# Performance work log

Hardware: AMD Instinct MI355X
Metric: run time of the kernel (lower is better)

## Reference

```python
import jax, jax.numpy as jnp
import numpy as np


def smooth_l1(x, y):
    d = jnp.abs(x - y)
    return jnp.where(d < 1.0, 0.5 * d * d, d - 0.5)


def setup_inputs() -> dict:
    key = jax.random.key(0)
    k1, k2, k3 = jax.random.split(key, 3)
    B, T, N, D = 4, 28, 1024, 3
    X_v = jax.random.normal(k1, (B, T, N, D), dtype=jnp.float32)
    target_X_v = jax.random.normal(k2, (B, T, N, D), dtype=jnp.float32)
    weights = jax.random.uniform(k3, (B, T), dtype=jnp.float32)
    return {"X_v": X_v, "target_X_v": target_X_v, "weights": weights}


def reference(X_v, target_X_v, weights):
    B = X_v.shape[0]
    # Pairwise squared distances [B,T,N,N] via ||p||^2 + ||t||^2 - 2 p.t
    pn = jnp.sum(X_v * X_v, axis=-1)                 # [B,T,N]
    tn = jnp.sum(target_X_v * target_X_v, axis=-1)   # [B,T,N]
    dist = (pn[..., :, None] + tn[..., None, :]
            - 2.0 * jnp.einsum('btnd,btmd->btnm', X_v, target_X_v))
    minv = jnp.argmin(dist, axis=-1)                 # [B,T,N] int
    # gather nearest target point for each pred point
    tagp = jnp.take_along_axis(target_X_v, minv[..., None], axis=2)  # [B,T,N,3]
    # per-(b,t) mean smooth-L1 over N points x 3 coords
    loss_bt = jnp.mean(smooth_l1(X_v, tagp), axis=(-2, -1))          # [B,T]
    loss = jnp.sum(loss_bt * weights) / B

    prec = jnp.mean(X_v, axis=2)        # [B,T,3]
    tarc = jnp.mean(target_X_v, axis=2) # [B,T,3]
    lossc = jnp.sum(smooth_l1(prec, tarc)) / (B * 3)
    return (loss, lossc)
```

## Files before the change

### kernel.cpp

```cpp
#include <hip/hip_runtime.h>

constexpr int Bc = 4;
constexpr int Tc = 28;
constexpr int Nc = 1024;
constexpr int Dc = 3;
constexpr int BT = Bc * Tc;
constexpr int QT = 256;

constexpr size_t WS_BESTV   = 0;
constexpr size_t WS_BESTI   = (size_t)BT * Nc * 4;
constexpr size_t WS_PARTIAL = WS_BESTI + (size_t)BT * Nc * 4;
constexpr size_t WS_PSUM    = WS_PARTIAL + 224;
constexpr size_t WS_TSUM    = WS_PSUM + BT * 2 * 3;

__device__ __forceinline__ float sl1(float d) {
    d = fabsf(d);
    return d < 1.0f ? 0.5f * d * d : d - 0.5f;
}

__global__ __launch_bounds__(256) void chamfer_quarter_kernel(
    const float* __restrict__ X, const float* __restrict__ Tg,
    float* __restrict__ bestv, int* __restrict__ besti,
    float* __restrict__ psum, float* __restrict__ tsum)
{
    __shared__ float4 sT4[QT];
    __shared__ float sred[4][3];

    const int bt  = blockIdx.x >> 3;
    const int ph  = (blockIdx.x >> 2) & 1;
    const int th  = blockIdx.x & 3;
    const int tid = threadIdx.x;

    const float* xb = X + (size_t)bt * (Nc * Dc);
    const int n0 = ph * 512 + tid;
    const int n1 = n0 + 256;
    const float pAx = xb[n0 * 3 + 0], pAy = xb[n0 * 3 + 1], pAz = xb[n0 * 3 + 2];
    const float pBx = xb[n1 * 3 + 0], pBy = xb[n1 * 3 + 1], pBz = xb[n1 * 3 + 2];

    if (tid < 64) {
        const float4* tg4 = (const float4*)(Tg + (size_t)bt * (Nc * Dc) + th * (QT * 3));
        const float4 r0 = tg4[3 * tid + 0];
        const float4 r1 = tg4[3 * tid + 1];
        const float4 r2 = tg4[3 * tid + 2];
        sT4[4 * tid + 0] = make_float4(r0.x, r0.y, r0.z, fmaf(r0.x, r0.x, fmaf(r0.y, r0.y, r0.z * r0.z)));
        sT4[4 * tid + 1] = make_float4(r0.w, r1.x, r1.y, fmaf(r0.w, r0.w, fmaf(r1.x, r1.x, r1.y * r1.y)));
        sT4[4 * tid + 2] = make_float4(r1.z, r1.w, r2.x, fmaf(r1.z, r1.z, fmaf(r1.w, r1.w, r2.x * r2.x)));
        sT4[4 * tid + 3] = make_float4(r2.y, r2.z, r2.w, fmaf(r2.y, r2.y, fmaf(r2.z, r2.z, r2.w * r2.w)));
        if (ph == 0) {
            float tx = r0.x + r0.w + r1.z + r2.y;
            float ty = r0.y + r1.x + r1.w + r2.z;
            float tz = r0.z + r1.y + r2.x + r2.w;
            #pragma unroll
            for (int off = 32; off; off >>= 1) {
                tx += __shfl_down(tx, off, 64);
                ty += __shfl_down(ty, off, 64);
                tz += __shfl_down(tz, off, 64);
            }
            if (tid == 0) {
                tsum[(bt * 4 + th) * 3 + 0] = tx;
                tsum[(bt * 4 + th) * 3 + 1] = ty;
                tsum[(bt * 4 + th) * 3 + 2] = tz;
            }
        }
    }
    __syncthreads();

    const float cA0 = -2.0f * pAx, cA1 = -2.0f * pAy, cA2 = -2.0f * pAz;
    const float cB0 = -2.0f * pBx, cB1 = -2.0f * pBy, cB2 = -2.0f * pBz;

    float bestA = 3.4e38f, bestB = 3.4e38f;
    int iA = 0, iB = 0;

    constexpr int PF = 8;
    float4 bufA[PF], bufB[PF];
    #pragma unroll
    for (int j = 0; j < PF; ++j) bufA[j] = sT4[j];

    for (int m0 = 0; m0 < QT; m0 += 2 * PF) {
        #pragma unroll
        for (int j = 0; j < PF; ++j) bufB[j] = sT4[m0 + PF + j];
        #pragma unroll
        for (int j = 0; j < PF; ++j) {
            const float4 t = bufA[j];
            const int m = m0 + j;
            float vA = fmaf(cA0, t.x, fmaf(cA1, t.y, fmaf(cA2, t.z, t.w)));
            float vB = fmaf(cB0, t.x, fmaf(cB1, t.y, fmaf(cB2, t.z, t.w)));
            bool ca = vA < bestA; bestA = ca ? vA : bestA; iA = ca ? m : iA;
            bool cb = vB < bestB; bestB = cb ? vB : bestB; iB = cb ? m : iB;
        }
        #pragma unroll
        for (int j = 0; j < PF; ++j) bufA[j] = sT4[(m0 + 2 * PF + j) & (QT - 1)];
        #pragma unroll
        for (int j = 0; j < PF; ++j) {
            const float4 t = bufB[j];
            const int m = m0 + PF + j;
            float vA = fmaf(cA0, t.x, fmaf(cA1, t.y, fmaf(cA2, t.z, t.w)));
            float vB = fmaf(cB0, t.x, fmaf(cB1, t.y, fmaf(cB2, t.z, t.w)));
            bool ca = vA < bestA; bestA = ca ? vA : bestA; iA = ca ? m : iA;
            bool cb = vB < bestB; bestB = cb ? vB : bestB; iB = cb ? m : iB;
        }
    }

    const size_t base = (size_t)bt * Nc;
    bestv[(base + n0) * 4 + th] = bestA;
    bestv[(base + n1) * 4 + th] = bestB;
    besti[(base + n0) * 4 + th] = th * QT + iA;
    besti[(base + n1) * 4 + th] = th * QT + iB;

    if (th == 0) {
        float sx = pAx + pBx, sy = pAy + pBy, sz = pAz + pBz;
        const int lane = tid & 63, wid = tid >> 6;
        #pragma unroll
        for (int off = 32; off; off >>= 1) {
            sx += __shfl_down(sx, off, 64);
            sy += __shfl_down(sy, off, 64);
            sz += __shfl_down(sz, off, 64);
        }
        if (lane == 0) { sred[wid][0] = sx; sred[wid][1] = sy; sred[wid][2] = sz; }
        __syncthreads();
        if (tid == 0) {
            #pragma unroll
            for (int k = 0; k < 3; ++k)
                psum[(bt * 2 + ph) * 3 + k] = sred[0][k] + sred[1][k] + sred[2][k] + sred[3][k];
        }
    }
}

__global__ __launch_bounds__(256) void gather_kernel(
    const float* __restrict__ X, const float* __restrict__ Tg,
    const float* __restrict__ W,
    const float4* __restrict__ bestv4, const int4* __restrict__ besti4,
    float* __restrict__ partial)
{
    __shared__ float sred[4];
    const int bt  = blockIdx.x >> 1;
    const int ph  = blockIdx.x & 1;
    const int tid = threadIdx.x;

    const float* xb = X  + (size_t)bt * (Nc * Dc);
    const float* tb = Tg + (size_t)bt * (Nc * Dc);
    const size_t base = (size_t)bt * Nc;

    float s = 0.0f;
    #pragma unroll
    for (int p = 0; p < 2; ++p) {
        const int n = ph * 512 + p * 256 + tid;
        const float4 bv = bestv4[base + n];
        const int4   bi = besti4[base + n];
        float best = bv.x; int idx = bi.x;
        if (bv.y < best) { best = bv.y; idx = bi.y; }
        if (bv.z < best) { best = bv.z; idx = bi.z; }
        if (bv.w < best) { best = bv.w; idx = bi.w; }
        const float px = xb[n * 3 + 0], py = xb[n * 3 + 1], pz = xb[n * 3 + 2];
        const float tx = tb[idx * 3 + 0], ty = tb[idx * 3 + 1], tz = tb[idx * 3 + 2];
        s += sl1(px - tx) + sl1(py - ty) + sl1(pz - tz);
    }

    const int lane = tid & 63, wid = tid >> 6;
    #pragma unroll
    for (int off = 32; off; off >>= 1) s += __shfl_down(s, off, 64);
    if (lane == 0) sred[wid] = s;
    __syncthreads();
    if (tid == 0)
        partial[blockIdx.x] = (sred[0] + sred[1] + sred[2] + sred[3]) * W[bt];
}

__global__ __launch_bounds__(256) void finalize_kernel(
    const float* __restrict__ ws, float* __restrict__ out)
{
    __shared__ float sred[4][2];
    const int tid = threadIdx.x;

    float lp = (tid < 224) ? ws[WS_PARTIAL + tid] : 0.0f;

    float lc = 0.0f;
    if (tid < BT) {
        const float inv = 1.0f / Nc;
        #pragma unroll
        for (int c = 0; c < 3; ++c) {
            float pm = (ws[WS_PSUM + (2 * tid) * 3 + c] + ws[WS_PSUM + (2 * tid + 1) * 3 + c]) * inv;
            float tm = (ws[WS_TSUM + (4 * tid) * 3 + c] + ws[WS_TSUM + (4 * tid + 1) * 3 + c]
                      + ws[WS_TSUM + (4 * tid + 2) * 3 + c] + ws[WS_TSUM + (4 * tid + 3) * 3 + c]) * inv;
            lc += sl1(pm - tm);
        }
    }

    const int lane = tid & 63, wid = tid >> 6;
    #pragma unroll
    for (int off = 32; off; off >>= 1) {
        lp += __shfl_down(lp, off, 64);
        lc += __shfl_down(lc, off, 64);
    }
    if (lane == 0) { sred[wid][0] = lp; sred[wid][1] = lc; }
    __syncthreads();
    if (tid == 0) {
        float tlp = sred[0][0] + sred[1][0] + sred[2][0] + sred[3][0];
        float tlc = sred[0][1] + sred[1][1] + sred[2][1] + sred[3][1];
        out[0] = tlp * (1.0f / (Nc * Dc)) * (1.0f / Bc);
        out[1] = tlc * (1.0f / (Bc * Dc));
    }
}

extern "C" void kernel_launch(void* const* d_in, const int* in_sizes, int n_in,
                              void* d_out, int out_size, void* d_ws, size_t ws_size,
                              hipStream_t stream) {
    const float* X  = (const float*)d_in[0];
    const float* Tg = (const float*)d_in[1];
    const float* W  = (const float*)d_in[2];
    float* out = (float*)d_out;
    float* ws  = (float*)d_ws;

    float* bestv = ws + WS_BESTV;
    int*   besti = (int*)(ws + WS_BESTI);
    float* psum  = ws + WS_PSUM;
    float* tsum  = ws + WS_TSUM;

    chamfer_quarter_kernel<<<BT * 8, 256, 0, stream>>>(X, Tg, bestv, besti, psum, tsum);
    gather_kernel<<<BT * 2, 256, 0, stream>>>(X, Tg, W,
        (const float4*)(ws + WS_BESTV), (const int4*)(ws + WS_BESTI), ws + WS_PARTIAL);
    finalize_kernel<<<1, 256, 0, stream>>>(ws, out);
}
```

Baseline: 88.72 us.

## Process four points per thread, merge gather and finalize with atomics

The chamfer kernel now gives each thread four consecutive predicted points, loaded as three float4s, instead of two strided points. This halves the block count and doubles reuse of each shared-memory target load. Partial results are stored per quarter in a layout suited to coalesced float4 reads. The gather and finalize kernels are merged into one, which accumulates the output through atomicAdd after a memset, removing one launch. The cost is fewer blocks (448), so lower occupancy and parallelism, plus more registers per thread and float atomics whose summation order is not deterministic.

```diff
diff --git a/kernel.cpp b/kernel.cpp
--- a/kernel.cpp
+++ b/kernel.cpp
@@ -6,36 +6,34 @@
 constexpr int Dc = 3;
 constexpr int BT = Bc * Tc;
 constexpr int QT = 256;
-
-constexpr size_t WS_BESTV   = 0;
-constexpr size_t WS_BESTI   = (size_t)BT * Nc * 4;
-constexpr size_t WS_PARTIAL = WS_BESTI + (size_t)BT * Nc * 4;
-constexpr size_t WS_PSUM    = WS_PARTIAL + 224;
-constexpr size_t WS_TSUM    = WS_PSUM + BT * 2 * 3;
+constexpr int NQ = 4;
+
+constexpr size_t WS_BESTV = 0;
+constexpr size_t WS_BESTI = (size_t)NQ * BT * 256 * 4;
+constexpr size_t WS_PSUM  = WS_BESTI + (size_t)NQ * BT * 256 * 4;
+constexpr size_t WS_TSUM  = WS_PSUM + BT * 3;
 
 __device__ __forceinline__ float sl1(float d) {
     d = fabsf(d);
     return d < 1.0f ? 0.5f * d * d : d - 0.5f;
 }
 
-__global__ __launch_bounds__(256) void chamfer_quarter_kernel(
+__global__ __launch_bounds__(256) void chamfer_kernel(
     const float* __restrict__ X, const float* __restrict__ Tg,
-    float* __restrict__ bestv, int* __restrict__ besti,
+    float4* __restrict__ bestvP, int4* __restrict__ bestiP,
     float* __restrict__ psum, float* __restrict__ tsum)
 {
     __shared__ float4 sT4[QT];
     __shared__ float sred[4][3];
 
-    const int bt  = blockIdx.x >> 3;
-    const int ph  = (blockIdx.x >> 2) & 1;
+    const int bt  = blockIdx.x >> 2;
     const int th  = blockIdx.x & 3;
     const int tid = threadIdx.x;
 
-    const float* xb = X + (size_t)bt * (Nc * Dc);
-    const int n0 = ph * 512 + tid;
-    const int n1 = n0 + 256;
-    const float pAx = xb[n0 * 3 + 0], pAy = xb[n0 * 3 + 1], pAz = xb[n0 * 3 + 2];
-    const float pBx = xb[n1 * 3 + 0], pBy = xb[n1 * 3 + 1], pBz = xb[n1 * 3 + 2];
+    const float4* x4 = (const float4*)(X + (size_t)bt * (Nc * Dc));
+    const float4 a0 = x4[3 * tid + 0];
+    const float4 a1 = x4[3 * tid + 1];
+    const float4 a2 = x4[3 * tid + 2];
 
     if (tid < 64) {
         const float4* tg4 = (const float4*)(Tg + (size_t)bt * (Nc * Dc) + th * (QT * 3));
@@ -46,32 +44,31 @@
         sT4[4 * tid + 1] = make_float4(r0.w, r1.x, r1.y, fmaf(r0.w, r0.w, fmaf(r1.x, r1.x, r1.y * r1.y)));
         sT4[4 * tid + 2] = make_float4(r1.z, r1.w, r2.x, fmaf(r1.z, r1.z, fmaf(r1.w, r1.w, r2.x * r2.x)));
         sT4[4 * tid + 3] = make_float4(r2.y, r2.z, r2.w, fmaf(r2.y, r2.y, fmaf(r2.z, r2.z, r2.w * r2.w)));
-        if (ph == 0) {
-            float tx = r0.x + r0.w + r1.z + r2.y;
-            float ty = r0.y + r1.x + r1.w + r2.z;
-            float tz = r0.z + r1.y + r2.x + r2.w;
-            #pragma unroll
-            for (int off = 32; off; off >>= 1) {
-                tx += __shfl_down(tx, off, 64);
-                ty += __shfl_down(ty, off, 64);
-                tz += __shfl_down(tz, off, 64);
-            }
-            if (tid == 0) {
-                tsum[(bt * 4 + th) * 3 + 0] = tx;
-                tsum[(bt * 4 + th) * 3 + 1] = ty;
-                tsum[(bt * 4 + th) * 3 + 2] = tz;
-            }
+        float tx = r0.x + r0.w + r1.z + r2.y;
+        float ty = r0.y + r1.x + r1.w + r2.z;
+        float tz = r0.z + r1.y + r2.x + r2.w;
+        #pragma unroll
+        for (int off = 32; off; off >>= 1) {
+            tx += __shfl_down(tx, off, 64);
+            ty += __shfl_down(ty, off, 64);
+            tz += __shfl_down(tz, off, 64);
+        }
+        if (tid == 0) {
+            tsum[(bt * NQ + th) * 3 + 0] = tx;
+            tsum[(bt * NQ + th) * 3 + 1] = ty;
+            tsum[(bt * NQ + th) * 3 + 2] = tz;
         }
     }
     __syncthreads();
 
-    const float cA0 = -2.0f * pAx, cA1 = -2.0f * pAy, cA2 = -2.0f * pAz;
-    const float cB0 = -2.0f * pBx, cB1 = -2.0f * pBy, cB2 = -2.0f * pBz;
-
-    float bestA = 3.4e38f, bestB = 3.4e38f;
-    int iA = 0, iB = 0;
-
-    constexpr int PF = 8;
+    const float c0[4] = {-2.f * a0.x, -2.f * a0.w, -2.f * a1.z, -2.f * a2.y};
+    const float c1[4] = {-2.f * a0.y, -2.f * a1.x, -2.f * a1.w, -2.f * a2.z};
+    const float c2[4] = {-2.f * a0.z, -2.f * a1.y, -2.f * a2.x, -2.f * a2.w};
+
+    float best[4] = {3.4e38f, 3.4e38f, 3.4e38f, 3.4e38f};
+    int idx[4] = {0, 0, 0, 0};
+
+    constexpr int PF = 4;
     float4 bufA[PF], bufB[PF];
     #pragma unroll
     for (int j = 0; j < PF; ++j) bufA[j] = sT4[j];
@@ -83,10 +80,11 @@
         for (int j = 0; j < PF; ++j) {
             const float4 t = bufA[j];
             const int m = m0 + j;
-            float vA = fmaf(cA0, t.x, fmaf(cA1, t.y, fmaf(cA2, t.z, t.w)));
-            float vB = fmaf(cB0, t.x, fmaf(cB1, t.y, fmaf(cB2, t.z, t.w)));
-            bool ca = vA < bestA; bestA = ca ? vA : bestA; iA = ca ? m : iA;
-            bool cb = vB < bestB; bestB = cb ? vB : bestB; iB = cb ? m : iB;
+            #pragma unroll
+            for (int k = 0; k < 4; ++k) {
+                float v = fmaf(c0[k], t.x, fmaf(c1[k], t.y, fmaf(c2[k], t.z, t.w)));
+                bool c = v < best[k]; best[k] = c ? v : best[k]; idx[k] = c ? m : idx[k];
+            }
         }
         #pragma unroll
         for (int j = 0; j < PF; ++j) bufA[j] = sT4[(m0 + 2 * PF + j) & (QT - 1)];
@@ -94,21 +92,23 @@
         for (int j = 0; j < PF; ++j) {
             const float4 t = bufB[j];
             const int m = m0 + PF + j;
-            float vA = fmaf(cA0, t.x, fmaf(cA1, t.y, fmaf(cA2, t.z, t.w)));
-            float vB = fmaf(cB0, t.x, fmaf(cB1, t.y, fmaf(cB2, t.z, t.w)));
-            bool ca = vA < bestA; bestA = ca ? vA : bestA; iA = ca ? m : iA;
-            bool cb = vB < bestB; bestB = cb ? vB : bestB; iB = cb ? m : iB;
-        }
-    }
-
-    const size_t base = (size_t)bt * Nc;
-    bestv[(base + n0) * 4 + th] = bestA;
-    bestv[(base + n1) * 4 + th] = bestB;
-    besti[(base + n0) * 4 + th] = th * QT + iA;
-    besti[(base + n1) * 4 + th] = th * QT + iB;
+            #pragma unroll
+            for (int k = 0; k < 4; ++k) {
+                float v = fmaf(c0[k], t.x, fmaf(c1[k], t.y, fmaf(c2[k], t.z, t.w)));
+                bool c = v < best[k]; best[k] = c ? v : best[k]; idx[k] = c ? m : idx[k];
+            }
+        }
+    }
+
+    const size_t ob = ((size_t)th * BT + bt) * 256 + tid;
+    bestvP[ob] = make_float4(best[0], best[1], best[2], best[3]);
+    bestiP[ob] = make_int4(th * QT + idx[0], th * QT + idx[1],
+                           th * QT + idx[2], th * QT + idx[3]);
 
     if (th == 0) {
-        float sx = pAx + pBx, sy = pAy + pBy, sz = pAz + pBz;
+        float sx = a0.x + a0.w + a1.z + a2.y;
+        float sy = a0.y + a1.x + a1.w + a2.z;
+        float sz = a0.z + a1.y + a2.x + a2.w;
         const int lane = tid & 63, wid = tid >> 6;
         #pragma unroll
         for (int off = 32; off; off >>= 1) {
@@ -121,39 +121,54 @@
         if (tid == 0) {
             #pragma unroll
             for (int k = 0; k < 3; ++k)
-                psum[(bt * 2 + ph) * 3 + k] = sred[0][k] + sred[1][k] + sred[2][k] + sred[3][k];
-        }
-    }
-}
-
-__global__ __launch_bounds__(256) void gather_kernel(
+                psum[bt * 3 + k] = sred[0][k] + sred[1][k] + sred[2][k] + sred[3][k];
+        }
+    }
+}
+
+__global__ __launch_bounds__(256) void gather_finalize_kernel(
     const float* __restrict__ X, const float* __restrict__ Tg,
     const float* __restrict__ W,
-    const float4* __restrict__ bestv4, const int4* __restrict__ besti4,
-    float* __restrict__ partial)
+    const float4* __restrict__ bestvP, const int4* __restrict__ bestiP,
+    const float* __restrict__ psum, const float* __restrict__ tsum,
+    float* __restrict__ out)
 {
     __shared__ float sred[4];
-    const int bt  = blockIdx.x >> 1;
-    const int ph  = blockIdx.x & 1;
+    __shared__ float sred2[4];
+    const int bt  = blockIdx.x;
     const int tid = threadIdx.x;
-
-    const float* xb = X  + (size_t)bt * (Nc * Dc);
+    const size_t rb = (size_t)bt * 256 + tid;
+
+    float4 bv = bestvP[rb];
+    int4   bi = bestiP[rb];
+    float best[4] = {bv.x, bv.y, bv.z, bv.w};
+    int   idx[4]  = {bi.x, bi.y, bi.z, bi.w};
+    #pragma unroll
+    for (int q = 1; q < NQ; ++q) {
+        const float4 v2 = bestvP[(size_t)q * BT * 256 + rb];
+        const int4   i2 = bestiP[(size_t)q * BT * 256 + rb];
+        if (v2.x < best[0]) { best[0] = v2.x; idx[0] = i2.x; }
+        if (v2.y < best[1]) { best[1] = v2.y; idx[1] = i2.y; }
+        if (v2.z < best[2]) { best[2] = v2.z; idx[2] = i2.z; }
+        if (v2.w < best[3]) { best[3] = v2.w; idx[3] = i2.w; }
+    }
+
     const float* tb = Tg + (size_t)bt * (Nc * Dc);
-    const size_t base = (size_t)bt * Nc;
+    const float4* x4 = (const float4*)(X + (size_t)bt * (Nc * Dc));
+    const float4 a0 = x4[3 * tid + 0];
+    const float4 a1 = x4[3 * tid + 1];
+    const float4 a2 = x4[3 * tid + 2];
+    const float px[4] = {a0.x, a0.w, a1.z, a2.y};
+    const float py[4] = {a0.y, a1.x, a1.w, a2.z};
+    const float pz[4] = {a0.z, a1.y, a2.x, a2.w};
 
     float s = 0.0f;
     #pragma unroll
-    for (int p = 0; p < 2; ++p) {
-        const int n = ph * 512 + p * 256 + tid;
-        const float4 bv = bestv4[base + n];
-        const int4   bi = besti4[base + n];
-        float best = bv.x; int idx = bi.x;
-        if (bv.y < best) { best = bv.y; idx = bi.y; }
-        if (bv.z < best) { best = bv.z; idx = bi.z; }
-        if (bv.w < best) { best = bv.w; idx = bi.w; }
-        const float px = xb[n * 3 + 0], py = xb[n * 3 + 1], pz = xb[n * 3 + 2];
-        const float tx = tb[idx * 3 + 0], ty = tb[idx * 3 + 1], tz = tb[idx * 3 + 2];
-        s += sl1(px - tx) + sl1(py - ty) + sl1(pz - tz);
+    for (int k = 0; k < 4; ++k) {
+        const float tx = tb[idx[k] * 3 + 0];
+        const float ty = tb[idx[k] * 3 + 1];
+        const float tz = tb[idx[k] * 3 + 2];
+        s += sl1(px[k] - tx) + sl1(py[k] - ty) + sl1(pz[k] - tz);
     }
 
     const int lane = tid & 63, wid = tid >> 6;
@@ -161,43 +176,32 @@
     for (int off = 32; off; off >>= 1) s += __shfl_down(s, off, 64);
     if (lane == 0) sred[wid] = s;
     __syncthreads();
-    if (tid == 0)
-        partial[blockIdx.x] = (sred[0] + sred[1] + sred[2] + sred[3]) * W[bt];
-}
-
-__global__ __launch_bounds__(256) void finalize_kernel(
-    const float* __restrict__ ws, float* __restrict__ out)
-{
-    __shared__ float sred[4][2];
-    const int tid = threadIdx.x;
-
-    float lp = (tid < 224) ? ws[WS_PARTIAL + tid] : 0.0f;
-
-    float lc = 0.0f;
-    if (tid < BT) {
-        const float inv = 1.0f / Nc;
-        #pragma unroll
-        for (int c = 0; c < 3; ++c) {
-            float pm = (ws[WS_PSUM + (2 * tid) * 3 + c] + ws[WS_PSUM + (2 * tid + 1) * 3 + c]) * inv;
-            float tm = (ws[WS_TSUM + (4 * tid) * 3 + c] + ws[WS_TSUM + (4 * tid + 1) * 3 + c]
-                      + ws[WS_TSUM + (4 * tid + 2) * 3 + c] + ws[WS_TSUM + (4 * tid + 3) * 3 + c]) * inv;
-            lc += sl1(pm - tm);
-        }
-    }
-
-    const int lane = tid & 63, wid = tid >> 6;
-    #pragma unroll
-    for (int off = 32; off; off >>= 1) {
-        lp += __shfl_down(lp, off, 64);
-        lc += __shfl_down(lc, off, 64);
-    }
-    if (lane == 0) { sred[wid][0] = lp; sred[wid][1] = lc; }
-    __syncthreads();
     if (tid == 0) {
-        float tlp = sred[0][0] + sred[1][0] + sred[2][0] + sred[3][0];
-        float tlc = sred[0][1] + sred[1][1] + sred[2][1] + sred[3][1];
-        out[0] = tlp * (1.0f / (Nc * Dc)) * (1.0f / Bc);
-        out[1] = tlc * (1.0f / (Bc * Dc));
+        float tot = sred[0] + sred[1] + sred[2] + sred[3];
+        atomicAdd(out, tot * W[bt] * (1.0f / (Nc * Dc)) * (1.0f / Bc));
+    }
+
+    if (bt == 0) {
+        float lc = 0.0f;
+        if (tid < BT) {
+            const float inv = 1.0f / Nc;
+            #pragma unroll
+            for (int c = 0; c < 3; ++c) {
+                float pm = psum[tid * 3 + c] * inv;
+                float tm = (tsum[(tid * NQ + 0) * 3 + c] + tsum[(tid * NQ + 1) * 3 + c]
+                          + tsum[(tid * NQ + 2) * 3 + c] + tsum[(tid * NQ + 3) * 3 + c]) * inv;
+                lc += sl1(pm - tm);
+            }
+        }
+        float v = lc;
+        #pragma unroll
+        for (int off = 32; off; off >>= 1) v += __shfl_down(v, off, 64);
+        if (lane == 0) sred2[wid] = v;
+        __syncthreads();
+        if (tid == 0) {
+            float tlc = sred2[0] + sred2[1] + sred2[2] + sred2[3];
+            atomicAdd(out + 1, tlc * (1.0f / (Bc * Dc)));
+        }
     }
 }
 
@@ -210,13 +214,12 @@
     float* out = (float*)d_out;
     float* ws  = (float*)d_ws;
 
-    float* bestv = ws + WS_BESTV;
-    int*   besti = (int*)(ws + WS_BESTI);
-    float* psum  = ws + WS_PSUM;
-    float* tsum  = ws + WS_TSUM;
-
-    chamfer_quarter_kernel<<<BT * 8, 256, 0, stream>>>(X, Tg, bestv, besti, psum, tsum);
-    gather_kernel<<<BT * 2, 256, 0, stream>>>(X, Tg, W,
-        (const float4*)(ws + WS_BESTV), (const int4*)(ws + WS_BESTI), ws + WS_PARTIAL);
-    finalize_kernel<<<1, 256, 0, stream>>>(ws, out);
-}
+    float4* bestvP = (float4*)(ws + WS_BESTV);
+    int4*   bestiP = (int4*)(ws + WS_BESTI);
+    float*  psum   = ws + WS_PSUM;
+    float*  tsum   = ws + WS_TSUM;
+
+    hipMemsetAsync(out, 0, 2 * sizeof(float), stream);
+    chamfer_kernel<<<BT * NQ, 256, 0, stream>>>(X, Tg, bestvP, bestiP, psum, tsum);
+    gather_finalize_kernel<<<BT, 256, 0, stream>>>(X, Tg, W, bestvP, bestiP, psum, tsum, out);
+}
```

New measurement: 85.61 us. -3.5%, faster.
